# Performance work log

Hardware: AMD Instinct MI355X
Metric: run time of the kernel (lower is better)

The kernel has to match this reference:

```python
import jax, jax.numpy as jnp
import numpy as np

PAIR_DIM = 128
HIDDEN_DIM = 128
N = 512
EPS = 1e-5


def _layer_norm(x, scale, bias):
    mu = jnp.mean(x, axis=-1, keepdims=True)
    var = jnp.var(x, axis=-1, keepdims=True)
    return (x - mu) * jax.lax.rsqrt(var + EPS) * scale + bias


def setup_inputs() -> dict:
    key = jax.random.key(0)
    ks = jax.random.split(key, 16)
    d, h = PAIR_DIM, HIDDEN_DIM
    s = lambda fan_in: 1.0 / np.sqrt(fan_in)
    inp = {
        "pair_embed": jax.random.normal(ks[0], (N, N, d), dtype=jnp.float32),
        "zn_scale": jnp.ones((d,), jnp.float32),
        "zn_bias": jnp.zeros((d,), jnp.float32),
        "ln_scale": jnp.ones((h,), jnp.float32),
        "ln_bias": jnp.zeros((h,), jnp.float32),
        "w_a": jax.random.uniform(ks[1], (d, h), jnp.float32, -s(d), s(d)),
        "b_a": jax.random.uniform(ks[2], (h,), jnp.float32, -s(d), s(d)),
        "w_ga": jax.random.uniform(ks[3], (d, h), jnp.float32, -s(d), s(d)),
        "b_ga": jax.random.uniform(ks[4], (h,), jnp.float32, -s(d), s(d)),
        "w_b": jax.random.uniform(ks[5], (d, h), jnp.float32, -s(d), s(d)),
        "b_b": jax.random.uniform(ks[6], (h,), jnp.float32, -s(d), s(d)),
        "w_gb": jax.random.uniform(ks[7], (d, h), jnp.float32, -s(d), s(d)),
        "b_gb": jax.random.uniform(ks[8], (h,), jnp.float32, -s(d), s(d)),
        "w_o": jax.random.uniform(ks[9], (h, d), jnp.float32, -s(h), s(h)),
        "b_o": jax.random.uniform(ks[10], (d,), jnp.float32, -s(h), s(h)),
        "w_g": jax.random.uniform(ks[11], (d, d), jnp.float32, -s(d), s(d)),
        "b_g": jax.random.uniform(ks[12], (d,), jnp.float32, -s(d), s(d)),
    }
    return inp


def reference(pair_embed, zn_scale, zn_bias, ln_scale, ln_bias,
              w_a, b_a, w_ga, b_ga, w_b, b_b, w_gb, b_gb,
              w_o, b_o, w_g, b_g):
    # z norm over pair channels
    z = _layer_norm(pair_embed, zn_scale, zn_bias)          # [N,N,d]
    node_1 = (z @ w_a + b_a) * jax.nn.sigmoid(z @ w_ga + b_ga)   # [N,N,h]
    node_2 = (z @ w_b + b_b) * jax.nn.sigmoid(z @ w_gb + b_gb)   # [N,N,h]
    # triangle multiply: contract over shared residue k, per channel h
    pair_update = jnp.einsum('ikh,jkh->ijh', node_1, node_2)     # [N,N,h]
    pair_update = _layer_norm(pair_update, ln_scale, ln_bias)
    pair_update = pair_update @ w_o + b_o                        # [N,N,d]
    gate_out = jax.nn.sigmoid(z @ w_g + b_g)
    return pair_update * gate_out
```

## Files before the change

kernel.cpp:

```cpp
#include <hip/hip_runtime.h>

#define NSEQ 512
#define DD 128
#define NP (NSEQ * NSEQ)

typedef unsigned short u16;
typedef __attribute__((ext_vector_type(8))) unsigned short u16x8;
typedef __attribute__((ext_vector_type(4))) unsigned short u16x4;
typedef __attribute__((ext_vector_type(8))) short bf16x8;
typedef __attribute__((ext_vector_type(4))) float f32x4;

__device__ __forceinline__ u16 f2bf(float f) {
  unsigned int x = __float_as_uint(f);
  return (u16)((x + 0x7fffu + ((x >> 16) & 1u)) >> 16);
}
__device__ __forceinline__ float bf2f(u16 u) {
  return __uint_as_float(((unsigned int)u) << 16);
}
__device__ __forceinline__ f32x4 mfma16(bf16x8 a, bf16x8 b, f32x4 c) {
  return __builtin_amdgcn_mfma_f32_16x16x32_bf16(a, b, c, 0, 0, 0);
}
__device__ __forceinline__ void gload16(const void* g, void* l) {
  __builtin_amdgcn_global_load_lds(
      (const __attribute__((address_space(1))) unsigned int*)g,
      (__attribute__((address_space(3))) unsigned int*)l, 16, 0, 0);
}
__device__ __forceinline__ float sigmoidf_(float v) { return 1.f / (1.f + __expf(-v)); }

__global__ void kW(const float* __restrict__ wa, const float* __restrict__ wga,
                   const float* __restrict__ wb, const float* __restrict__ wgb,
                   const float* __restrict__ wg, const float* __restrict__ wo,
                   u16* __restrict__ Wp) {
  int b = blockIdx.x, t = threadIdx.x;
  int m = b >> 5, cf = (b >> 2) & 7, kf = b & 3;
  const float* m6[6] = {wa, wga, wb, wgb, wg, wo};
  const float* src = m6[m];
  int lane = t >> 1, e0 = (t & 1) * 4;
  u16* dst = Wp + m * 16384 + (cf * 4 + kf) * 512 + lane * 8 + e0;
  int col = cf * 16 + (lane & 15);
  int row0 = kf * 32 + (lane >> 4) * 8 + e0;
#pragma unroll
  for (int e = 0; e < 4; ++e) dst[e] = f2bf(src[(row0 + e) * 128 + col]);
}

__global__ void __launch_bounds__(256)
    __attribute__((amdgpu_waves_per_eu(4, 4)))
    kA(const float* __restrict__ x, const float* __restrict__ zn_s,
       const float* __restrict__ zn_b, const float* __restrict__ b_a,
       const float* __restrict__ b_ga, const float* __restrict__ b_b,
       const float* __restrict__ b_gb, const u16* __restrict__ Wp,
       u16* __restrict__ n1t, u16* __restrict__ n2t) {
  __shared__ __align__(16) u16 z[128 * 136];
  int tid = threadIdx.x;
  int pos0 = blockIdx.x * 128;
  int lane = tid & 63, w = tid >> 6;

  {
    int r = tid >> 1, hf = tid & 1;
    const float* px = x + (size_t)pos0 * 128 + r * 128 + hf * 64;
    float4 xv[16];
    float s = 0.f, s2 = 0.f;
#pragma unroll
    for (int q = 0; q < 16; ++q) {
      xv[q] = *(const float4*)(px + q * 4);
      s += xv[q].x + xv[q].y + xv[q].z + xv[q].w;
      s2 += xv[q].x * xv[q].x + xv[q].y * xv[q].y + xv[q].z * xv[q].z + xv[q].w * xv[q].w;
    }
    s += __shfl_xor(s, 1);
    s2 += __shfl_xor(s2, 1);
    float mu = s * (1.f / 128.f);
    float rs = rsqrtf(s2 * (1.f / 128.f) - mu * mu + 1e-5f);
#pragma unroll
    for (int q = 0; q < 16; ++q) {
      int c0 = hf * 64 + q * 4;
      u16x4 o;
      o[0] = f2bf((xv[q].x - mu) * rs * zn_s[c0 + 0] + zn_b[c0 + 0]);
      o[1] = f2bf((xv[q].y - mu) * rs * zn_s[c0 + 1] + zn_b[c0 + 1]);
      o[2] = f2bf((xv[q].z - mu) * rs * zn_s[c0 + 2] + zn_b[c0 + 2]);
      o[3] = f2bf((xv[q].w - mu) * rs * zn_s[c0 + 3] + zn_b[c0 + 3]);
      *(u16x4*)&z[r * 136 + c0] = o;
    }
  }
  __syncthreads();

  bf16x8 af[2][4];
#pragma unroll
  for (int rf = 0; rf < 2; ++rf)
#pragma unroll
    for (int kf = 0; kf < 4; ++kf)
      af[rf][kf] = *(const bf16x8*)&z[(w * 32 + rf * 16 + (lane & 15)) * 136 + kf * 32 + (lane >> 4) * 8];

  int colL = lane & 15;

#pragma unroll 1
  for (int g = 0; g < 2; ++g) {
    const float* bxp = g ? b_b : b_a;
    const float* bgp = g ? b_gb : b_ga;
    u16* dst = g ? n2t : n1t;
    const u16* WxP = Wp + (g * 2) * 16384 + lane * 8;
    const u16* WgP = Wp + (g * 2 + 1) * 16384 + lane * 8;

    bf16x8 wxf[2][4], wgf[2][4];
#pragma unroll
    for (int kf = 0; kf < 4; ++kf) {
      wxf[0][kf] = *(const bf16x8*)&WxP[kf * 512];
      wgf[0][kf] = *(const bf16x8*)&WgP[kf * 512];
    }

#pragma unroll
    for (int cf = 0; cf < 8; ++cf) {
      int cb = cf & 1, nb = cb ^ 1;
      if (cf < 7) {
#pragma unroll
        for (int kf = 0; kf < 4; ++kf) {
          wxf[nb][kf] = *(const bf16x8*)&WxP[((cf + 1) * 4 + kf) * 512];
          wgf[nb][kf] = *(const bf16x8*)&WgP[((cf + 1) * 4 + kf) * 512];
        }
      }
      f32x4 ax0 = {0.f, 0.f, 0.f, 0.f}, ax1 = ax0, ag0 = ax0, ag1 = ax0;
#pragma unroll
      for (int kf = 0; kf < 4; ++kf) {
        ax0 = mfma16(af[0][kf], wxf[cb][kf], ax0);
        ax1 = mfma16(af[1][kf], wxf[cb][kf], ax1);
        ag0 = mfma16(af[0][kf], wgf[cb][kf], ag0);
        ag1 = mfma16(af[1][kf], wgf[cb][kf], ag1);
      }
      int h = cf * 16 + colL;
      float bx_ = bxp[h], bg_ = bgp[h];
      size_t hb = (size_t)h * NP + pos0 + w * 32 + (lane >> 4) * 4;
      u16x4 o0, o1;
#pragma unroll
      for (int r = 0; r < 4; ++r) {
        o0[r] = f2bf((ax0[r] + bx_) * sigmoidf_(ag0[r] + bg_));
        o1[r] = f2bf((ax1[r] + bx_) * sigmoidf_(ag1[r] + bg_));
      }
      *(u16x4*)&dst[hb] = o0;
      *(u16x4*)&dst[hb + 16] = o1;
    }
  }
}

__global__ __launch_bounds__(256) void kB(const u16* __restrict__ n1t,
                                          const u16* __restrict__ n2t,
                                          u16* __restrict__ P) {
  __shared__ __align__(16) u16 At[2][128 * 64];
  __shared__ __align__(16) u16 Bt[2][128 * 64];
  int bid = blockIdx.x;
  int h = bid >> 4, t = bid & 15;
  int i0 = (t >> 2) * 128, j0 = (t & 3) * 128;
  const u16* Ab = n1t + (size_t)h * NP + (size_t)i0 * 512;
  const u16* Bb = n2t + (size_t)h * NP + (size_t)j0 * 512;
  int tid = threadIdx.x, lane = tid & 63, w = tid >> 6;

  f32x4 acc[4][4];
#pragma unroll
  for (int a_ = 0; a_ < 4; ++a_)
#pragma unroll
    for (int b_ = 0; b_ < 4; ++b_) acc[a_][b_] = f32x4{0.f, 0.f, 0.f, 0.f};

  auto STAGE = [&](int buf, int kt) {
#pragma unroll
    for (int q = 0; q < 4; ++q) {
      int c = q * 256 + tid;
      int row = c >> 3, ch = c & 7;
      int chG = ch ^ (row & 7);
      gload16(Ab + (size_t)row * 512 + kt * 64 + chG * 8, &At[buf][c * 8]);
    }
#pragma unroll
    for (int q = 0; q < 4; ++q) {
      int c = q * 256 + tid;
      int row = c >> 3, ch = c & 7;
      int chG = ch ^ (row & 7);
      gload16(Bb + (size_t)row * 512 + kt * 64 + chG * 8, &Bt[buf][c * 8]);
    }
  };

  STAGE(0, 0);
  int cur = 0;
  int r0 = (w >> 1) * 64, c0 = (w & 1) * 64;
#pragma unroll 1
  for (int kt = 0; kt < 8; ++kt) {
    if (kt < 7) {
      STAGE(cur ^ 1, kt + 1);
      __builtin_amdgcn_sched_barrier(0);
      asm volatile("s_waitcnt vmcnt(8)" ::: "memory");
    } else {
      asm volatile("s_waitcnt vmcnt(0)" ::: "memory");
    }
    __builtin_amdgcn_sched_barrier(0);
    __builtin_amdgcn_s_barrier();
    __builtin_amdgcn_sched_barrier(0);
#pragma unroll
    for (int kf = 0; kf < 2; ++kf) {
      bf16x8 a[4], b[4];
#pragma unroll
      for (int rf = 0; rf < 4; ++rf) {
        int row = r0 + rf * 16 + (lane & 15);
        a[rf] = *(const bf16x8*)&At[cur][row * 64 + (((kf * 4 + (lane >> 4)) ^ (row & 7)) * 8)];
      }
#pragma unroll
      for (int cf = 0; cf < 4; ++cf) {
        int row = c0 + cf * 16 + (lane & 15);
        b[cf] = *(const bf16x8*)&Bt[cur][row * 64 + (((kf * 4 + (lane >> 4)) ^ (row & 7)) * 8)];
      }
#pragma unroll
      for (int rf = 0; rf < 4; ++rf)
#pragma unroll
        for (int cf = 0; cf < 4; ++cf) acc[rf][cf] = mfma16(a[rf], b[cf], acc[rf][cf]);
    }
    __builtin_amdgcn_sched_barrier(0);
    __builtin_amdgcn_s_barrier();
    __builtin_amdgcn_sched_barrier(0);
    cur ^= 1;
  }

  size_t Pb = (size_t)h * NP;
#pragma unroll
  for (int rf = 0; rf < 4; ++rf)
#pragma unroll
    for (int cf = 0; cf < 4; ++cf) {
      int ii = i0 + (w >> 1) * 64 + rf * 16 + (lane >> 4) * 4;
      int jj = j0 + (w & 1) * 64 + cf * 16 + (lane & 15);
#pragma unroll
      for (int r = 0; r < 4; ++r) P[Pb + (size_t)(ii + r) * 512 + jj] = f2bf(acc[rf][cf][r]);
    }
}

__global__ void __launch_bounds__(256)
    __attribute__((amdgpu_waves_per_eu(4, 4)))
    kC(const float* __restrict__ x, const u16* __restrict__ P,
       const float* __restrict__ zn_s, const float* __restrict__ zn_b,
       const float* __restrict__ ln_s, const float* __restrict__ ln_b,
       const u16* __restrict__ Wp, const float* __restrict__ b_o,
       const float* __restrict__ b_g, float* __restrict__ out) {
  __shared__ __align__(16) u16 T[128 * 136];
  int tid = threadIdx.x, lane = tid & 63, w = tid >> 6;
  int i = blockIdx.x >> 2, jb = blockIdx.x & 3;
  size_t pos0 = (size_t)i * 512 + jb * 128;

  {
    int r = tid >> 1, hf = tid & 1;
    const float* px = x + pos0 * 128 + r * 128 + hf * 64;
    float4 xv[16];
    float s = 0.f, s2 = 0.f;
#pragma unroll
    for (int q = 0; q < 16; ++q) {
      xv[q] = *(const float4*)(px + q * 4);
      s += xv[q].x + xv[q].y + xv[q].z + xv[q].w;
      s2 += xv[q].x * xv[q].x + xv[q].y * xv[q].y + xv[q].z * xv[q].z + xv[q].w * xv[q].w;
    }
    s += __shfl_xor(s, 1);
    s2 += __shfl_xor(s2, 1);
    float mu = s * (1.f / 128.f);
    float rs = rsqrtf(s2 * (1.f / 128.f) - mu * mu + 1e-5f);
#pragma unroll
    for (int q = 0; q < 16; ++q) {
      int c0 = hf * 64 + q * 4;
      u16x4 o;
      o[0] = f2bf((xv[q].x - mu) * rs * zn_s[c0 + 0] + zn_b[c0 + 0]);
      o[1] = f2bf((xv[q].y - mu) * rs * zn_s[c0 + 1] + zn_b[c0 + 1]);
      o[2] = f2bf((xv[q].z - mu) * rs * zn_s[c0 + 2] + zn_b[c0 + 2]);
      o[3] = f2bf((xv[q].w - mu) * rs * zn_s[c0 + 3] + zn_b[c0 + 3]);
      *(u16x4*)&T[r * 136 + c0] = o;
    }
  }
  __syncthreads();
  bf16x8 az[2][4];
#pragma unroll
  for (int rf = 0; rf < 2; ++rf)
#pragma unroll
    for (int kf = 0; kf < 4; ++kf)
      az[rf][kf] = *(const bf16x8*)&T[(w * 32 + rf * 16 + (lane & 15)) * 136 + kf * 32 + (lane >> 4) * 8];
  __syncthreads();

  {
    int sh = tid & 15, sj = tid >> 4;
    const u16* src = P + (size_t)(sh * 8) * NP + pos0 + sj * 8;
    u16x8 vv[8];
#pragma unroll
    for (int e = 0; e < 8; ++e) vv[e] = *(const u16x8*)(src + (size_t)e * NP);
#pragma unroll
    for (int f = 0; f < 8; ++f) {
      u16x8 ww;
#pragma unroll
      for (int e = 0; e < 8; ++e) ww[e] = vv[e][f];
      *(u16x8*)&T[(sj * 8 + f) * 136 + sh * 8] = ww;
    }
  }
  __syncthreads();

  {
    int r = tid >> 1, hf = tid & 1;
    u16x8 vq[8];
    float s = 0.f, s2 = 0.f;
#pragma unroll
    for (int q = 0; q < 8; ++q) {
      vq[q] = *(const u16x8*)&T[r * 136 + hf * 64 + q * 8];
#pragma unroll
      for (int e = 0; e < 8; ++e) {
        float f = bf2f(vq[q][e]);
        s += f;
        s2 += f * f;
      }
    }
    s += __shfl_xor(s, 1);
    s2 += __shfl_xor(s2, 1);
    float mu = s * (1.f / 128.f);
    float rs = rsqrtf(s2 * (1.f / 128.f) - mu * mu + 1e-5f);
#pragma unroll
    for (int q = 0; q < 8; ++q) {
      u16x8 o;
#pragma unroll
      for (int e = 0; e < 8; ++e) {
        int hh = hf * 64 + q * 8 + e;
        o[e] = f2bf((bf2f(vq[q][e]) - mu) * rs * ln_s[hh] + ln_b[hh]);
      }
      *(u16x8*)&T[r * 136 + hf * 64 + q * 8] = o;
    }
  }
  __syncthreads();

  bf16x8 ap[2][4];
#pragma unroll
  for (int rf = 0; rf < 2; ++rf)
#pragma unroll
    for (int kf = 0; kf < 4; ++kf)
      ap[rf][kf] = *(const bf16x8*)&T[(w * 32 + rf * 16 + (lane & 15)) * 136 + kf * 32 + (lane >> 4) * 8];

  const u16* WgP = Wp + 4 * 16384 + lane * 8;
  const u16* WoP = Wp + 5 * 16384 + lane * 8;

#pragma unroll 1
  for (int sub = 0; sub < 4; ++sub) {
    f32x4 au[2][2], agg[2][2];
#pragma unroll
    for (int rf = 0; rf < 2; ++rf)
#pragma unroll
      for (int cf = 0; cf < 2; ++cf) {
        au[rf][cf] = f32x4{0.f, 0.f, 0.f, 0.f};
        agg[rf][cf] = f32x4{0.f, 0.f, 0.f, 0.f};
      }
#pragma unroll
    for (int cf = 0; cf < 2; ++cf) {
      int cg = sub * 2 + cf;
#pragma unroll
      for (int kf = 0; kf < 4; ++kf) {
        bf16x8 bo_f = *(const bf16x8*)&WoP[(cg * 4 + kf) * 512];
        bf16x8 bg_f = *(const bf16x8*)&WgP[(cg * 4 + kf) * 512];
#pragma unroll
        for (int rf = 0; rf < 2; ++rf) {
          au[rf][cf] = mfma16(ap[rf][kf], bo_f, au[rf][cf]);
          agg[rf][cf] = mfma16(az[rf][kf], bg_f, agg[rf][cf]);
        }
      }
    }
#pragma unroll
    for (int rf = 0; rf < 2; ++rf)
#pragma unroll
      for (int cf = 0; cf < 2; ++cf) {
        int d = sub * 32 + cf * 16 + (lane & 15);
        float bo_ = b_o[d], bg_ = b_g[d];
        int jl = w * 32 + rf * 16 + (lane >> 4) * 4;
#pragma unroll
        for (int r = 0; r < 4; ++r) {
          float uv = au[rf][cf][r] + bo_;
          out[(pos0 + jl + r) * 128 + d] = uv * sigmoidf_(agg[rf][cf][r] + bg_);
        }
      }
  }
}

extern "C" void kernel_launch(void* const* d_in, const int* in_sizes, int n_in,
                              void* d_out, int out_size, void* d_ws, size_t ws_size,
                              hipStream_t stream) {
  const float* x = (const float*)d_in[0];
  const float* zn_s = (const float*)d_in[1];
  const float* zn_b = (const float*)d_in[2];
  const float* ln_s = (const float*)d_in[3];
  const float* ln_b = (const float*)d_in[4];
  const float* w_a = (const float*)d_in[5];
  const float* b_a = (const float*)d_in[6];
  const float* w_ga = (const float*)d_in[7];
  const float* b_ga = (const float*)d_in[8];
  const float* w_b = (const float*)d_in[9];
  const float* b_b = (const float*)d_in[10];
  const float* w_gb = (const float*)d_in[11];
  const float* b_gb = (const float*)d_in[12];
  const float* w_o = (const float*)d_in[13];
  const float* b_o = (const float*)d_in[14];
  const float* w_g = (const float*)d_in[15];
  const float* b_g = (const float*)d_in[16];

  char* ws = (char*)d_ws;
  u16* n1t = (u16*)ws;
  u16* n2t = (u16*)(ws + 67108864);
  u16* P = (u16*)(ws + 134217728);
  u16* Wp = (u16*)(ws + 201326592);

  kW<<<192, 128, 0, stream>>>(w_a, w_ga, w_b, w_gb, w_g, w_o, Wp);
  kA<<<2048, 256, 0, stream>>>(x, zn_s, zn_b, b_a, b_ga, b_b, b_gb, Wp, n1t, n2t);
  kB<<<2048, 256, 0, stream>>>(n1t, n2t, P);
  kC<<<2048, 256, 0, stream>>>(x, P, zn_s, zn_b, ln_s, ln_b, Wp, b_o, b_g, (float*)d_out);
}
```

Measured before the change: 306.8 us.

## Swap projection MFMA operand roles so weights stay in registers per wave

Reorganizes the input projection kernel so each wave owns two 16-channel output column groups and keeps their weight fragments and biases in registers, streaming z rows from LDS as the second operand instead of holding z fragments and reloading all weights from global memory per column group. This cuts repeated global weight loads and the double-buffer bookkeeping. In exchange, the transposed output is now written as scalar 2-byte stores at consecutive positions per lane group rather than 8-byte vector stores, which may hurt store efficiency.

```diff
diff --git a/kernel.cpp b/kernel.cpp
--- a/kernel.cpp
+++ b/kernel.cpp
@@ -83,14 +83,7 @@
   }
   __syncthreads();
 
-  bf16x8 af[2][4];
-#pragma unroll
-  for (int rf = 0; rf < 2; ++rf)
-#pragma unroll
-    for (int kf = 0; kf < 4; ++kf)
-      af[rf][kf] = *(const bf16x8*)&z[(w * 32 + rf * 16 + (lane & 15)) * 136 + kf * 32 + (lane >> 4) * 8];
-
-  int colL = lane & 15;
+  int quad = lane >> 4, colL = lane & 15;
 
 #pragma unroll 1
   for (int g = 0; g < 2; ++g) {
@@ -101,41 +94,47 @@
     const u16* WgP = Wp + (g * 2 + 1) * 16384 + lane * 8;
 
     bf16x8 wxf[2][4], wgf[2][4];
-#pragma unroll
-    for (int kf = 0; kf < 4; ++kf) {
-      wxf[0][kf] = *(const bf16x8*)&WxP[kf * 512];
-      wgf[0][kf] = *(const bf16x8*)&WgP[kf * 512];
-    }
-
-#pragma unroll
-    for (int cf = 0; cf < 8; ++cf) {
-      int cb = cf & 1, nb = cb ^ 1;
-      if (cf < 7) {
-#pragma unroll
-        for (int kf = 0; kf < 4; ++kf) {
-          wxf[nb][kf] = *(const bf16x8*)&WxP[((cf + 1) * 4 + kf) * 512];
-          wgf[nb][kf] = *(const bf16x8*)&WgP[((cf + 1) * 4 + kf) * 512];
-        }
-      }
-      f32x4 ax0 = {0.f, 0.f, 0.f, 0.f}, ax1 = ax0, ag0 = ax0, ag1 = ax0;
+    float bx[2][4], bg[2][4];
+#pragma unroll
+    for (int c2 = 0; c2 < 2; ++c2) {
+      int cf = w * 2 + c2;
 #pragma unroll
       for (int kf = 0; kf < 4; ++kf) {
-        ax0 = mfma16(af[0][kf], wxf[cb][kf], ax0);
-        ax1 = mfma16(af[1][kf], wxf[cb][kf], ax1);
-        ag0 = mfma16(af[0][kf], wgf[cb][kf], ag0);
-        ag1 = mfma16(af[1][kf], wgf[cb][kf], ag1);
-      }
-      int h = cf * 16 + colL;
-      float bx_ = bxp[h], bg_ = bgp[h];
-      size_t hb = (size_t)h * NP + pos0 + w * 32 + (lane >> 4) * 4;
-      u16x4 o0, o1;
+        wxf[c2][kf] = *(const bf16x8*)&WxP[(cf * 4 + kf) * 512];
+        wgf[c2][kf] = *(const bf16x8*)&WgP[(cf * 4 + kf) * 512];
+      }
 #pragma unroll
       for (int r = 0; r < 4; ++r) {
-        o0[r] = f2bf((ax0[r] + bx_) * sigmoidf_(ag0[r] + bg_));
-        o1[r] = f2bf((ax1[r] + bx_) * sigmoidf_(ag1[r] + bg_));
-      }
-      *(u16x4*)&dst[hb] = o0;
-      *(u16x4*)&dst[hb + 16] = o1;
+        int h = cf * 16 + quad * 4 + r;
+        bx[c2][r] = bxp[h];
+        bg[c2][r] = bgp[h];
+      }
+    }
+
+#pragma unroll 1
+    for (int n = 0; n < 8; ++n) {
+      bf16x8 zb[4];
+#pragma unroll
+      for (int kf = 0; kf < 4; ++kf)
+        zb[kf] = *(const bf16x8*)&z[(n * 16 + colL) * 136 + kf * 32 + quad * 8];
+      f32x4 au0 = {0.f, 0.f, 0.f, 0.f}, au1 = au0, ag0 = au0, ag1 = au0;
+#pragma unroll
+      for (int kf = 0; kf < 4; ++kf) {
+        au0 = mfma16(wxf[0][kf], zb[kf], au0);
+        au1 = mfma16(wxf[1][kf], zb[kf], au1);
+        ag0 = mfma16(wgf[0][kf], zb[kf], ag0);
+        ag1 = mfma16(wgf[1][kf], zb[kf], ag1);
+      }
+      int pos = pos0 + n * 16 + colL;
+#pragma unroll
+      for (int r = 0; r < 4; ++r) {
+        int h0 = (w * 2) * 16 + quad * 4 + r;
+        int h1 = (w * 2 + 1) * 16 + quad * 4 + r;
+        float v0 = (au0[r] + bx[0][r]) * sigmoidf_(ag0[r] + bg[0][r]);
+        float v1 = (au1[r] + bx[1][r]) * sigmoidf_(ag1[r] + bg[1][r]);
+        dst[(size_t)h0 * NP + pos] = f2bf(v0);
+        dst[(size_t)h1 * NP + pos] = f2bf(v1);
+      }
     }
   }
 }
```

New measurement: 283.7 us. 7.5% less time.
